# Optimization experiments

Hardware: AMD Instinct MI355X
Metric: run time of the kernel (lower is better)

The kernel has to match this reference:

```python
import jax, jax.numpy as jnp
import numpy as np

H = 128
N_CAN = 100000
N_FLAG = 50000
E = 600000
L = 500000


def _sage_conv(x_src, x_dst, edge_index, Wl, bl, Wr):
    # PyG SAGEConv (mean aggr): lin_l(mean_{j in N(i)} x_j) + lin_r(x_i)
    src, dst = edge_index[0], edge_index[1]
    msg = x_src[src]                                        # [E, H] gather
    n_dst = x_dst.shape[0]
    agg = jax.ops.segment_sum(msg, dst, num_segments=n_dst)  # [N_dst, H]
    cnt = jax.ops.segment_sum(jnp.ones((msg.shape[0],), msg.dtype), dst,
                              num_segments=n_dst)
    mean = agg / jnp.maximum(cnt, 1.0)[:, None]
    return mean @ Wl.T + bl + x_dst @ Wr.T


def setup_inputs() -> dict:
    key = jax.random.key(0)
    ks = jax.random.split(key, 16)
    s = 1.0 / np.sqrt(H)
    inp = {
        'can_node_id': jnp.arange(N_CAN, dtype=jnp.int64) if jax.config.jax_enable_x64 else jnp.arange(N_CAN, dtype=jnp.int32),
        'flag_node_id': jnp.arange(N_FLAG, dtype=jnp.int32),
        'edge_index_cf': jnp.stack([
            jax.random.randint(ks[0], (E,), 0, N_CAN),
            jax.random.randint(ks[1], (E,), 0, N_FLAG)]),
        'edge_index_fc': jnp.stack([
            jax.random.randint(ks[2], (E,), 0, N_FLAG),
            jax.random.randint(ks[3], (E,), 0, N_CAN)]),
        'edge_label_index': jnp.stack([
            jax.random.randint(ks[4], (L,), 0, N_CAN),
            jax.random.randint(ks[5], (L,), 0, N_FLAG)]),
        'can_emb': jax.random.normal(ks[6], (N_CAN, H), jnp.float32),
        'flag_emb': jax.random.normal(ks[7], (N_FLAG, H), jnp.float32),
        # SAGEConv for edge type CAN->flag (updates flag nodes)
        'Wl_cf': jax.random.normal(ks[8], (H, H), jnp.float32) * s,
        'bl_cf': jnp.zeros((H,), jnp.float32),
        'Wr_cf': jax.random.normal(ks[9], (H, H), jnp.float32) * s,
        # SAGEConv for edge type flag->CAN (updates CAN nodes)
        'Wl_fc': jax.random.normal(ks[10], (H, H), jnp.float32) * s,
        'bl_fc': jnp.zeros((H,), jnp.float32),
        'Wr_fc': jax.random.normal(ks[11], (H, H), jnp.float32) * s,
        # classifier MLP
        'W1': jax.random.normal(ks[12], (H, 2 * H), jnp.float32) * (1.0 / np.sqrt(2 * H)),
        'b1': jnp.zeros((H,), jnp.float32),
        'W2': jax.random.normal(ks[13], (1, H), jnp.float32) * s,
        'b2': jnp.zeros((1,), jnp.float32),
    }
    return inp


def reference(can_node_id, flag_node_id, edge_index_cf, edge_index_fc,
              edge_label_index, can_emb, flag_emb,
              Wl_cf, bl_cf, Wr_cf, Wl_fc, bl_fc, Wr_fc,
              W1, b1, W2, b2):
    # embedding lookups
    x_can = can_emb[can_node_id]    # [N_CAN, H]
    x_flag = flag_emb[flag_node_id]  # [N_FLAG, H]
    # to_hetero single SAGE layer + relu (dropout is identity in eval)
    upd_flag = jax.nn.relu(_sage_conv(x_can, x_flag, edge_index_cf, Wl_cf, bl_cf, Wr_cf))
    upd_can = jax.nn.relu(_sage_conv(x_flag, x_can, edge_index_fc, Wl_fc, bl_fc, Wr_fc))
    # link prediction classifier
    src = upd_can[edge_label_index[0]]   # [L, H]
    dst = upd_flag[edge_label_index[1]]  # [L, H]
    h = jax.nn.relu(jnp.concatenate([src, dst], axis=-1) @ W1.T + b1)
    out = h @ W2.T + b2
    return out.reshape(-1)
```

## Files before the change

### kernel.cpp

```cpp
#include <hip/hip_runtime.h>
#include <hip/hip_bf16.h>

#define H 128
#define BSH 8
#define MAXB 1024
#define PCH 4096
#define PIT (PCH / 256)

typedef __attribute__((ext_vector_type(8))) short short8;
typedef __attribute__((ext_vector_type(4))) short short4v;
typedef __attribute__((ext_vector_type(4))) float floatx4;
typedef unsigned short ushort_t;
typedef unsigned int uint_t;

__device__ __forceinline__ short f2bf(float f) {
    __hip_bfloat16 h = __float2bfloat16(f);
    return *reinterpret_cast<short*>(&h);
}
__device__ __forceinline__ float bflo(uint_t u) { return __uint_as_float(u << 16); }
__device__ __forceinline__ float bfhi(uint_t u) { return __uint_as_float(u & 0xFFFF0000u); }
__device__ __forceinline__ uint_t pack_bf2(float x, float y) {
    return (uint_t)(ushort_t)f2bf(x) | ((uint_t)(ushort_t)f2bf(y) << 16);
}
__device__ __forceinline__ void acc8(float* acc, uint4 r) {
    acc[0] += bflo(r.x); acc[1] += bfhi(r.x);
    acc[2] += bflo(r.y); acc[3] += bfhi(r.y);
    acc[4] += bflo(r.z); acc[5] += bfhi(r.z);
    acc[6] += bflo(r.w); acc[7] += bfhi(r.w);
}

__global__ __launch_bounds__(256)
void bucket_hist_cvt_kernel(const int* __restrict__ ei1, const int* __restrict__ ei2,
                            int E, int NF, int B, int* __restrict__ bcnt, int nbh,
                            const float* __restrict__ a, int n4a,
                            const float* __restrict__ b, int n4b,
                            ushort_t* __restrict__ da, ushort_t* __restrict__ db,
                            const float* __restrict__ Wl_cf, const float* __restrict__ Wr_cf,
                            const float* __restrict__ Wl_fc, const float* __restrict__ Wr_fc,
                            const float* __restrict__ W1, ushort_t* __restrict__ wb) {
    __shared__ int h[MAXB];
    int tid = threadIdx.x;
    if ((int)blockIdx.x < nbh) {
        for (int i = tid; i < B; i += 256) h[i] = 0;
        __syncthreads();
        int base = blockIdx.x * PCH;
        #pragma unroll 4
        for (int it = 0; it < PIT; ++it) {
            int t = base + it * 256 + tid;
            if (t < 2 * E) {
                int g = (t < E) ? ei1[E + t] : (ei2[E + t - E] + NF);
                atomicAdd(&h[g >> BSH], 1);
            }
        }
        __syncthreads();
        for (int i = tid; i < B; i += 256)
            if (h[i]) atomicAdd(&bcnt[i], h[i]);
        return;
    }
    int i = ((int)blockIdx.x - nbh) * 256 + tid;
    const float* src; ushort_t* dst; int k;
    if (i < n4a) { src = a; dst = da; k = i; }
    else if (i < n4a + n4b) { src = b; dst = db; k = i - n4a; }
    else {
        int idx = (i - n4a - n4b) * 4;
        if (idx >= 98304) return;
        int off;
        if      (idx < 16384) { src = Wl_cf; off = idx; }
        else if (idx < 32768) { src = Wr_cf; off = idx - 16384; }
        else if (idx < 49152) { src = Wl_fc; off = idx - 32768; }
        else if (idx < 65536) { src = Wr_fc; off = idx - 49152; }
        else                  { src = W1;    off = idx - 65536; }
        float4 v = *(const float4*)(src + off);
        short4v s;
        s[0] = f2bf(v.x); s[1] = f2bf(v.y); s[2] = f2bf(v.z); s[3] = f2bf(v.w);
        *(short4v*)(wb + idx) = s;
        return;
    }
    float4 v = ((const float4*)src)[k];
    short4v s;
    s[0] = f2bf(v.x); s[1] = f2bf(v.y); s[2] = f2bf(v.z); s[3] = f2bf(v.w);
    ((short4v*)dst)[k] = s;
}

__global__ __launch_bounds__(256)
void partition_kernel(const int* __restrict__ ei1, const int* __restrict__ ei2,
                      int E, int NF, int B, const int* __restrict__ bcnt,
                      int* __restrict__ bfront, uint_t* __restrict__ part) {
    __shared__ int h[MAXB];
    __shared__ int basex[MAXB];
    __shared__ int sdata[256];
    int tid = threadIdx.x;
    {
        int base4 = tid * 4;
        int v[4]; int s = 0;
        #pragma unroll
        for (int i = 0; i < 4; ++i) { int idx = base4 + i; v[i] = (idx < B) ? bcnt[idx] : 0; s += v[i]; }
        sdata[tid] = s;
        __syncthreads();
        for (int off = 1; off < 256; off <<= 1) {
            int t = (tid >= off) ? sdata[tid - off] : 0;
            __syncthreads();
            sdata[tid] += t;
            __syncthreads();
        }
        int excl = tid ? sdata[tid - 1] : 0;
        #pragma unroll
        for (int i = 0; i < 4; ++i) {
            int idx = base4 + i;
            if (idx < B) basex[idx] = excl;
            excl += v[i];
        }
    }
    for (int i = tid; i < B; i += 256) h[i] = 0;
    __syncthreads();

    int base = blockIdx.x * PCH;
    int pay[PIT]; int bkv[PIT]; int rv[PIT];
    #pragma unroll
    for (int it = 0; it < PIT; ++it) {
        int t = base + it * 256 + tid;
        bkv[it] = -1;
        if (t < 2 * E) {
            int g, s;
            if (t < E) { g = ei1[E + t]; s = ei1[t]; }
            else       { int e = t - E; g = ei2[E + e] + NF; s = ei2[e]; }
            int bk = g >> BSH;
            bkv[it] = bk;
            rv[it] = atomicAdd(&h[bk], 1);
            pay[it] = (int)(((uint_t)(g & 255) << 24) | (uint_t)s);
        }
    }
    __syncthreads();
    for (int i = tid; i < B; i += 256) {
        int c = h[i];
        if (c) basex[i] += atomicAdd(&bfront[i], c);
    }
    __syncthreads();
    #pragma unroll
    for (int it = 0; it < PIT; ++it) {
        if (bkv[it] >= 0)
            part[basex[bkv[it]] + rv[it]] = (uint_t)pay[it];
    }
}

__global__ __launch_bounds__(256)
void fine_bin_kernel(const int* __restrict__ bcnt, int B, int nTot, int E2,
                     const uint_t* __restrict__ part,
                     int* __restrict__ offs, int* __restrict__ bins) {
    __shared__ int cnt[256];
    __shared__ int sdata[256];
    __shared__ int excl[256];
    int b = blockIdx.x;
    int tid = threadIdx.x;
    {
        int partial = 0;
        for (int i = tid; i < b; i += 256) partial += bcnt[i];
        sdata[tid] = partial;
        __syncthreads();
        for (int off = 128; off > 0; off >>= 1) {
            if (tid < off) sdata[tid] += sdata[tid + off];
            __syncthreads();
        }
    }
    int seg0 = sdata[0];
    int seg1 = seg0 + bcnt[b];
    int gbase = b << BSH;
    __syncthreads();
    cnt[tid] = 0;
    __syncthreads();
    for (int k = seg0 + tid; k < seg1; k += 256)
        atomicAdd(&cnt[part[k] >> 24], 1);
    __syncthreads();
    sdata[tid] = cnt[tid];
    __syncthreads();
    for (int off = 1; off < 256; off <<= 1) {
        int t = (tid >= off) ? sdata[tid - off] : 0;
        __syncthreads();
        sdata[tid] += t;
        __syncthreads();
    }
    excl[tid] = tid ? sdata[tid - 1] : 0;
    int g = gbase + tid;
    if (g < nTot) offs[g] = seg0 + excl[tid];
    if (b == 0 && tid == 0) offs[nTot] = E2;
    cnt[tid] = 0;
    __syncthreads();
    for (int k = seg0 + tid; k < seg1; k += 256) {
        uint_t e = part[k];
        int l = (int)(e >> 24);
        int r = atomicAdd(&cnt[l], 1);
        bins[seg0 + excl[l] + r] = (int)(e & 0x00FFFFFFu);
    }
}

__global__ __launch_bounds__(256)
void gather_mean16_kernel(const int* __restrict__ offs, int nTotal, int split,
                          const int* __restrict__ bins,
                          const ushort_t* __restrict__ embA, ushort_t* __restrict__ aggA,
                          const ushort_t* __restrict__ embB, ushort_t* __restrict__ aggB) {
    int g = blockIdx.x * 16 + (threadIdx.x >> 4);
    if (g >= nTotal) return;
    int l15 = threadIdx.x & 15;
    int start = offs[g];
    int end = offs[g + 1];
    int deg = end - start;
    const ushort_t* emb; ushort_t* agg; int row;
    if (g < split) { emb = embA; agg = aggA; row = g; }
    else           { emb = embB; agg = aggB; row = g - split; }

    float acc[8];
    #pragma unroll
    for (int t = 0; t < 8; ++t) acc[t] = 0.f;

    const ushort_t* ep = emb + l15 * 8;
    int nPre = deg < 16 ? deg : 16;
    int pre = (l15 < nPre) ? bins[start + l15] : 0;

    int k = 0;
    for (; k + 3 < nPre; k += 4) {
        int s0 = __shfl(pre, k,     16);
        int s1 = __shfl(pre, k + 1, 16);
        int s2 = __shfl(pre, k + 2, 16);
        int s3 = __shfl(pre, k + 3, 16);
        uint4 r0 = *(const uint4*)(ep + (size_t)s0 * H);
        uint4 r1 = *(const uint4*)(ep + (size_t)s1 * H);
        uint4 r2 = *(const uint4*)(ep + (size_t)s2 * H);
        uint4 r3 = *(const uint4*)(ep + (size_t)s3 * H);
        acc8(acc, r0); acc8(acc, r1); acc8(acc, r2); acc8(acc, r3);
    }
    for (; k < nPre; ++k) {
        int s = __shfl(pre, k, 16);
        uint4 r = *(const uint4*)(ep + (size_t)s * H);
        acc8(acc, r);
    }
    for (int kk = start + 16; kk < end; ++kk) {
        int s = bins[kk];
        uint4 r = *(const uint4*)(ep + (size_t)s * H);
        acc8(acc, r);
    }

    float inv = 1.0f / fmaxf((float)deg, 1.0f);
    uint4 o;
    o.x = pack_bf2(acc[0] * inv, acc[1] * inv);
    o.y = pack_bf2(acc[2] * inv, acc[3] * inv);
    o.z = pack_bf2(acc[4] * inv, acc[5] * inv);
    o.w = pack_bf2(acc[6] * inv, acc[7] * inv);
    *(uint4*)(agg + (size_t)row * H + l15 * 8) = o;
}

__global__ __launch_bounds__(256)
void sage3_kernel(int nbF, int NF, int NC,
                  ushort_t* __restrict__ aggf, const ushort_t* __restrict__ embf,
                  ushort_t* __restrict__ aggc, const ushort_t* __restrict__ embc,
                  const ushort_t* __restrict__ wlf, const ushort_t* __restrict__ wrf,
                  const float* __restrict__ blf,
                  const ushort_t* __restrict__ wlc, const ushort_t* __restrict__ wrc,
                  const float* __restrict__ blc,
                  const ushort_t* __restrict__ W1) {
    __shared__ short A[64][136];
    bool isF = (int)blockIdx.x < nbF;
    int nrows = isF ? NF : NC;
    int rbase = (isF ? blockIdx.x : blockIdx.x - nbF) * 64;
    ushort_t* io = isF ? aggf : aggc;
    const ushort_t* emb = isF ? embf : embc;
    const ushort_t* Wl = isF ? wlf : wlc;
    const ushort_t* Wr = isF ? wrf : wrc;
    const float* bl = isF ? blf : blc;
    int koff = isF ? 128 : 0;

    int tid = threadIdx.x;
    int lane = tid & 63;
    int wv = tid >> 6;
    int l15 = lane & 15;
    int quad = lane >> 4;
    int nb0 = 32 * wv + l15;

    floatx4 acc[4][2];
    #pragma unroll
    for (int i = 0; i < 4; ++i)
        #pragma unroll
        for (int j = 0; j < 2; ++j)
            acc[i][j] = (floatx4){0.f, 0.f, 0.f, 0.f};

    float blv0 = bl[nb0];
    float blv1 = bl[nb0 + 16];

    for (int idx = tid; idx < 64 * 16; idx += 256) {
        int r = idx >> 4, c = idx & 15;
        int row = rbase + r;
        uint4 v = (uint4){0u, 0u, 0u, 0u};
        if (row < nrows) v = *(const uint4*)(io + (size_t)row * H + c * 8);
        *(uint4*)&A[r][c * 8] = v;
    }
    __syncthreads();
    #pragma unroll
    for (int ks = 0; ks < 4; ++ks) {
        int kb = ks * 32 + quad * 8;
        short8 b0 = *(const short8*)(Wl + (size_t)nb0 * H + kb);
        short8 b1 = *(const short8*)(Wl + (size_t)(nb0 + 16) * H + kb);
        #pragma unroll
        for (int mt = 0; mt < 4; ++mt) {
            short8 a = *(const short8*)&A[16 * mt + l15][kb];
            acc[mt][0] = __builtin_amdgcn_mfma_f32_16x16x32_bf16(a, b0, acc[mt][0], 0, 0, 0);
            acc[mt][1] = __builtin_amdgcn_mfma_f32_16x16x32_bf16(a, b1, acc[mt][1], 0, 0, 0);
        }
    }
    __syncthreads();

    for (int idx = tid; idx < 64 * 16; idx += 256) {
        int r = idx >> 4, c = idx & 15;
        int row = rbase + r;
        uint4 v = (uint4){0u, 0u, 0u, 0u};
        if (row < nrows) v = *(const uint4*)(emb + (size_t)row * H + c * 8);
        *(uint4*)&A[r][c * 8] = v;
    }
    __syncthreads();
    #pragma unroll
    for (int ks = 0; ks < 4; ++ks) {
        int kb = ks * 32 + quad * 8;
        short8 b0 = *(const short8*)(Wr + (size_t)nb0 * H + kb);
        short8 b1 = *(const short8*)(Wr + (size_t)(nb0 + 16) * H + kb);
        #pragma unroll
        for (int mt = 0; mt < 4; ++mt) {
            short8 a = *(const short8*)&A[16 * mt + l15][kb];
            acc[mt][0] = __builtin_amdgcn_mfma_f32_16x16x32_bf16(a, b0, acc[mt][0], 0, 0, 0);
            acc[mt][1] = __builtin_amdgcn_mfma_f32_16x16x32_bf16(a, b1, acc[mt][1], 0, 0, 0);
        }
    }
    __syncthreads();

    #pragma unroll
    for (int mt = 0; mt < 4; ++mt)
        #pragma unroll
        for (int nt = 0; nt < 2; ++nt) {
            float blv = nt ? blv1 : blv0;
            int colw = nb0 + 16 * nt;
            #pragma unroll
            for (int rg = 0; rg < 4; ++rg) {
                int row = 16 * mt + quad * 4 + rg;
                A[row][colw] = f2bf(fmaxf(acc[mt][nt][rg] + blv, 0.0f));
                acc[mt][nt][rg] = 0.0f;
            }
        }
    __syncthreads();

    const ushort_t* W1p = W1 + koff;
    #pragma unroll
    for (int ks = 0; ks < 4; ++ks) {
        int kb = ks * 32 + quad * 8;
        short8 b0 = *(const short8*)(W1p + (size_t)nb0 * 256 + kb);
        short8 b1 = *(const short8*)(W1p + (size_t)(nb0 + 16) * 256 + kb);
        #pragma unroll
        for (int mt = 0; mt < 4; ++mt) {
            short8 a = *(const short8*)&A[16 * mt + l15][kb];
            acc[mt][0] = __builtin_amdgcn_mfma_f32_16x16x32_bf16(a, b0, acc[mt][0], 0, 0, 0);
            acc[mt][1] = __builtin_amdgcn_mfma_f32_16x16x32_bf16(a, b1, acc[mt][1], 0, 0, 0);
        }
    }

    #pragma unroll
    for (int mt = 0; mt < 4; ++mt)
        #pragma unroll
        for (int rg = 0; rg < 4; ++rg) {
            int row = rbase + 16 * mt + quad * 4 + rg;
            if (row < nrows) {
                io[(size_t)row * H + nb0]      = (ushort_t)f2bf(acc[mt][0][rg]);
                io[(size_t)row * H + nb0 + 16] = (ushort_t)f2bf(acc[mt][1][rg]);
            }
        }
}

__global__ __launch_bounds__(256)
void hist2_kernel(const int* __restrict__ ei1, const int* __restrict__ ei2, int E,
                  int* __restrict__ deg1, int* __restrict__ deg2) {
    int t = blockIdx.x * 256 + threadIdx.x;
    if (t < E) atomicAdd(&deg1[ei1[E + t]], 1);
    else if (t < 2 * E) { int e = t - E; atomicAdd(&deg2[ei2[E + e]], 1); }
}

__global__ __launch_bounds__(256)
void scan_blocksum_kernel(const int* __restrict__ deg, int n, int* __restrict__ bsums) {
    __shared__ int sdata[256];
    int tid = threadIdx.x;
    int base = blockIdx.x * 1024 + tid * 4;
    int v = 0;
    #pragma unroll
    for (int i = 0; i < 4; ++i) { int idx = base + i; if (idx < n) v += deg[idx]; }
    sdata[tid] = v;
    __syncthreads();
    for (int off = 128; off > 0; off >>= 1) {
        if (tid < off) sdata[tid] += sdata[tid + off];
        __syncthreads();
    }
    if (tid == 0) bsums[blockIdx.x] = sdata[0];
}

__global__ __launch_bounds__(256)
void scan_write_kernel(int* __restrict__ data, int n, const int* __restrict__ bsums) {
    __shared__ int sdata[256];
    __shared__ int boff;
    int tid = threadIdx.x;
    if (tid < 64) {
        int acc = 0;
        for (int i = tid; i < (int)blockIdx.x; i += 64) acc += bsums[i];
        #pragma unroll
        for (int off = 32; off > 0; off >>= 1) acc += __shfl_xor(acc, off, 64);
        if (tid == 0) boff = acc;
    }
    int base = blockIdx.x * 1024 + tid * 4;
    int v[4]; int s = 0;
    #pragma unroll
    for (int i = 0; i < 4; ++i) { int idx = base + i; v[i] = (idx < n) ? data[idx] : 0; s += v[i]; }
    sdata[tid] = s;
    __syncthreads();
    for (int off = 1; off < 256; off <<= 1) {
        int t = (tid >= off) ? sdata[tid - off] : 0;
        __syncthreads();
        sdata[tid] += t;
        __syncthreads();
    }
    int excl = (tid == 0 ? 0 : sdata[tid - 1]) + boff;
    #pragma unroll
    for (int i = 0; i < 4; ++i) {
        int idx = base + i;
        if (idx < n) data[idx] = excl;
        excl += v[i];
    }
}

__global__ __launch_bounds__(256)
void incl_to_start_kernel(const int* __restrict__ incl, int nTot, int* __restrict__ offs) {
    int g = blockIdx.x * 256 + threadIdx.x;
    if (g < nTot) offs[g + 1] = incl[g];
    if (g == 0) offs[0] = 0;
}

__global__ __launch_bounds__(256)
void bin2_kernel(const int* __restrict__ ei1, const int* __restrict__ ei2, int E,
                 int* __restrict__ offs1, int* __restrict__ offs2,
                 int* __restrict__ bins) {
    int t = blockIdx.x * 256 + threadIdx.x;
    if (t < E) {
        int pos = atomicAdd(&offs1[ei1[E + t]], 1);
        bins[pos] = ei1[t];
    } else if (t < 2 * E) {
        int e = t - E;
        int pos = atomicAdd(&offs2[ei2[E + e]], 1);
        bins[pos] = ei2[e];
    }
}

__global__ __launch_bounds__(256)
void classify_kernel(const int* __restrict__ eli, int L,
                     const ushort_t* __restrict__ u_can,
                     const ushort_t* __restrict__ u_flag,
                     const float* __restrict__ b1,
                     const float* __restrict__ W2,
                     const float* __restrict__ b2,
                     float* __restrict__ out) {
    int tid = threadIdx.x;
    int lane = tid & 63;
    int wv = tid >> 6;
    int sub = lane >> 4;
    int l15 = lane & 15;
    int p = blockIdx.x * 16 + wv * 4 + sub;
    if (p >= L) return;
    int i = eli[p];
    int j = eli[L + p];
    uint4 a = ((const uint4*)(u_can  + (size_t)i * H))[l15];
    uint4 b = ((const uint4*)(u_flag + (size_t)j * H))[l15];
    float4 bb0 = ((const float4*)b1)[l15 * 2];
    float4 bb1 = ((const float4*)b1)[l15 * 2 + 1];
    float4 w0  = ((const float4*)W2)[l15 * 2];
    float4 w1  = ((const float4*)W2)[l15 * 2 + 1];
    float s = fmaxf(bflo(a.x) + bflo(b.x) + bb0.x, 0.f) * w0.x
            + fmaxf(bfhi(a.x) + bfhi(b.x) + bb0.y, 0.f) * w0.y
            + fmaxf(bflo(a.y) + bflo(b.y) + bb0.z, 0.f) * w0.z
            + fmaxf(bfhi(a.y) + bfhi(b.y) + bb0.w, 0.f) * w0.w
            + fmaxf(bflo(a.z) + bflo(b.z) + bb1.x, 0.f) * w1.x
            + fmaxf(bfhi(a.z) + bfhi(b.z) + bb1.y, 0.f) * w1.y
            + fmaxf(bflo(a.w) + bflo(b.w) + bb1.z, 0.f) * w1.z
            + fmaxf(bfhi(a.w) + bfhi(b.w) + bb1.w, 0.f) * w1.w;
    #pragma unroll
    for (int off = 8; off > 0; off >>= 1)
        s += __shfl_down(s, off, 16);
    if (l15 == 0) out[p] = s + b2[0];
}

extern "C" void kernel_launch(void* const* d_in, const int* in_sizes, int n_in,
                              void* d_out, int out_size, void* d_ws, size_t ws_size,
                              hipStream_t stream) {
    const int*   ei_cf    = (const int*)d_in[2];
    const int*   ei_fc    = (const int*)d_in[3];
    const int*   eli      = (const int*)d_in[4];
    const float* can_emb  = (const float*)d_in[5];
    const float* flag_emb = (const float*)d_in[6];
    const float* Wl_cf    = (const float*)d_in[7];
    const float* bl_cf    = (const float*)d_in[8];
    const float* Wr_cf    = (const float*)d_in[9];
    const float* Wl_fc    = (const float*)d_in[10];
    const float* bl_fc    = (const float*)d_in[11];
    const float* Wr_fc    = (const float*)d_in[12];
    const float* W1       = (const float*)d_in[13];
    const float* b1       = (const float*)d_in[14];
    const float* W2       = (const float*)d_in[15];
    const float* b2       = (const float*)d_in[16];
    float* out = (float*)d_out;

    const int NCAN  = in_sizes[0];
    const int NFLAG = in_sizes[1];
    const int E     = in_sizes[2] / 2;
    const int L     = in_sizes[4] / 2;
    const int nTot  = NCAN + NFLAG;
    const int B     = (nTot + 255) >> BSH;

    ushort_t* aggc = (ushort_t*)d_ws;
    ushort_t* aggf = aggc + (size_t)NCAN * H;
    ushort_t* embc = aggf + (size_t)NFLAG * H;
    ushort_t* embf = embc + (size_t)NCAN * H;
    char* tail = (char*)(embf + (size_t)NFLAG * H);
    size_t tail_off = (size_t)(tail - (char*)d_ws);

    int nbF = (NFLAG + 63) / 64, nbC = (NCAN + 63) / 64;
    int n4c = NCAN * H / 4, n4f = NFLAG * H / 4;
    int nbcvt = (n4c + n4f + 24576 + 255) / 256;

    size_t off_offs  = tail_off;
    size_t off_bcnt  = off_offs  + (size_t)(nTot + 1) * 4;
    size_t off_bfrnt = off_bcnt  + (size_t)MAXB * 4;
    size_t off_bins  = off_bfrnt + (size_t)MAXB * 4;
    size_t off_part  = off_bins  + (size_t)2 * E * 4;
    size_t off_wb    = off_part  + (size_t)2 * E * 4;
    size_t need_new  = off_wb + 98304 * 2;

    int* offs   = (int*)((char*)d_ws + off_offs);
    int* bcnt   = (int*)((char*)d_ws + off_bcnt);
    int* bfront = (int*)((char*)d_ws + off_bfrnt);
    int* bins   = (int*)((char*)d_ws + off_bins);

    if (ws_size >= need_new && B <= MAXB) {
        uint_t* part = (uint_t*)((char*)d_ws + off_part);
        ushort_t* wb = (ushort_t*)((char*)d_ws + off_wb);
        ushort_t* wb_wlcf = wb, *wb_wrcf = wb + 16384, *wb_wlfc = wb + 32768,
                 *wb_wrfc = wb + 49152, *wb_w1 = wb + 65536;

        int nbh = (2 * E + PCH - 1) / PCH;
        hipMemsetAsync(bcnt, 0, (size_t)2 * MAXB * 4, stream);
        bucket_hist_cvt_kernel<<<nbh + nbcvt, 256, 0, stream>>>(
            ei_cf, ei_fc, E, NFLAG, B, bcnt, nbh,
            can_emb, n4c, flag_emb, n4f, embc, embf,
            Wl_cf, Wr_cf, Wl_fc, Wr_fc, W1, wb);
        partition_kernel<<<nbh, 256, 0, stream>>>(ei_cf, ei_fc, E, NFLAG, B, bcnt, bfront, part);
        fine_bin_kernel<<<B, 256, 0, stream>>>(bcnt, B, nTot, 2 * E, part, offs, bins);
        gather_mean16_kernel<<<(nTot + 15) / 16, 256, 0, stream>>>(
            offs, nTot, NFLAG, bins, embc, aggf, embf, aggc);
        sage3_kernel<<<nbF + nbC, 256, 0, stream>>>(
            nbF, NFLAG, NCAN, aggf, embf, aggc, embc,
            wb_wlcf, wb_wrcf, bl_cf, wb_wlfc, wb_wrfc, bl_fc, wb_w1);
    } else {
        int* scanf_ = bins;
        int* scanc_ = scanf_ + NFLAG;
        int* bins2  = scanc_ + NCAN;
        int* bsums  = bins2 + 2 * E;
        ushort_t* wb = (ushort_t*)(bsums + 256);
        ushort_t* wb_wlcf = wb, *wb_wrcf = wb + 16384, *wb_wlfc = wb + 32768,
                 *wb_wrfc = wb + 49152, *wb_w1 = wb + 65536;

        bucket_hist_cvt_kernel<<<nbcvt, 256, 0, stream>>>(
            ei_cf, ei_fc, E, NFLAG, B, bcnt, 0,
            can_emb, n4c, flag_emb, n4f, embc, embf,
            Wl_cf, Wr_cf, Wl_fc, Wr_fc, W1, wb);
        hipMemsetAsync(scanf_, 0, ((size_t)NFLAG + NCAN) * 4, stream);
        int nb = (nTot + 1023) / 1024;
        hist2_kernel<<<(2 * E + 255) / 256, 256, 0, stream>>>(ei_cf, ei_fc, E, scanf_, scanc_);
        scan_blocksum_kernel<<<nb, 256, 0, stream>>>(scanf_, nTot, bsums);
        scan_write_kernel<<<nb, 256, 0, stream>>>(scanf_, nTot, bsums);
        bin2_kernel<<<(2 * E + 255) / 256, 256, 0, stream>>>(ei_cf, ei_fc, E, scanf_, scanc_, bins2);
        incl_to_start_kernel<<<(nTot + 255) / 256, 256, 0, stream>>>(scanf_, nTot, offs);
        gather_mean16_kernel<<<(nTot + 15) / 16, 256, 0, stream>>>(
            offs, nTot, NFLAG, bins2, embc, aggf, embf, aggc);
        sage3_kernel<<<nbF + nbC, 256, 0, stream>>>(
            nbF, NFLAG, NCAN, aggf, embf, aggc, embc,
            wb_wlcf, wb_wrcf, bl_cf, wb_wlfc, wb_wrfc, bl_fc, wb_w1);
    }

    classify_kernel<<<(L + 15) / 16, 256, 0, stream>>>(
        eli, L, aggc, aggf, b1, W2, b2, out);
}
```

Before: 308.7 us.

## Fuse neighbor mean aggregation into SAGE GEMM kernel via shared memory

Removes the separate gather_mean16 kernel. Each sage block now gathers and averages neighbor embeddings for its own 64 rows and writes the bf16 means straight into shared memory before the MFMA GEMM. This drops a kernel launch and the global write and re-read of the aggregated tensor. In exchange, the gather runs with a block count of only N/64 and feeds the GEMM phase directly, which may cut latency hiding for the irregular gathers.

```diff
diff --git a/kernel.cpp b/kernel.cpp
--- a/kernel.cpp
+++ b/kernel.cpp
@@ -194,64 +194,10 @@
 }
 
 __global__ __launch_bounds__(256)
-void gather_mean16_kernel(const int* __restrict__ offs, int nTotal, int split,
-                          const int* __restrict__ bins,
-                          const ushort_t* __restrict__ embA, ushort_t* __restrict__ aggA,
-                          const ushort_t* __restrict__ embB, ushort_t* __restrict__ aggB) {
-    int g = blockIdx.x * 16 + (threadIdx.x >> 4);
-    if (g >= nTotal) return;
-    int l15 = threadIdx.x & 15;
-    int start = offs[g];
-    int end = offs[g + 1];
-    int deg = end - start;
-    const ushort_t* emb; ushort_t* agg; int row;
-    if (g < split) { emb = embA; agg = aggA; row = g; }
-    else           { emb = embB; agg = aggB; row = g - split; }
-
-    float acc[8];
-    #pragma unroll
-    for (int t = 0; t < 8; ++t) acc[t] = 0.f;
-
-    const ushort_t* ep = emb + l15 * 8;
-    int nPre = deg < 16 ? deg : 16;
-    int pre = (l15 < nPre) ? bins[start + l15] : 0;
-
-    int k = 0;
-    for (; k + 3 < nPre; k += 4) {
-        int s0 = __shfl(pre, k,     16);
-        int s1 = __shfl(pre, k + 1, 16);
-        int s2 = __shfl(pre, k + 2, 16);
-        int s3 = __shfl(pre, k + 3, 16);
-        uint4 r0 = *(const uint4*)(ep + (size_t)s0 * H);
-        uint4 r1 = *(const uint4*)(ep + (size_t)s1 * H);
-        uint4 r2 = *(const uint4*)(ep + (size_t)s2 * H);
-        uint4 r3 = *(const uint4*)(ep + (size_t)s3 * H);
-        acc8(acc, r0); acc8(acc, r1); acc8(acc, r2); acc8(acc, r3);
-    }
-    for (; k < nPre; ++k) {
-        int s = __shfl(pre, k, 16);
-        uint4 r = *(const uint4*)(ep + (size_t)s * H);
-        acc8(acc, r);
-    }
-    for (int kk = start + 16; kk < end; ++kk) {
-        int s = bins[kk];
-        uint4 r = *(const uint4*)(ep + (size_t)s * H);
-        acc8(acc, r);
-    }
-
-    float inv = 1.0f / fmaxf((float)deg, 1.0f);
-    uint4 o;
-    o.x = pack_bf2(acc[0] * inv, acc[1] * inv);
-    o.y = pack_bf2(acc[2] * inv, acc[3] * inv);
-    o.z = pack_bf2(acc[4] * inv, acc[5] * inv);
-    o.w = pack_bf2(acc[6] * inv, acc[7] * inv);
-    *(uint4*)(agg + (size_t)row * H + l15 * 8) = o;
-}
-
-__global__ __launch_bounds__(256)
-void sage3_kernel(int nbF, int NF, int NC,
-                  ushort_t* __restrict__ aggf, const ushort_t* __restrict__ embf,
-                  ushort_t* __restrict__ aggc, const ushort_t* __restrict__ embc,
+void sage4_kernel(int nbF, int NF, int NC,
+                  const int* __restrict__ offs, const int* __restrict__ bins,
+                  ushort_t* __restrict__ outf, const ushort_t* __restrict__ embf,
+                  ushort_t* __restrict__ outc, const ushort_t* __restrict__ embc,
                   const ushort_t* __restrict__ wlf, const ushort_t* __restrict__ wrf,
                   const float* __restrict__ blf,
                   const ushort_t* __restrict__ wlc, const ushort_t* __restrict__ wrc,
@@ -261,12 +207,14 @@
     bool isF = (int)blockIdx.x < nbF;
     int nrows = isF ? NF : NC;
     int rbase = (isF ? blockIdx.x : blockIdx.x - nbF) * 64;
-    ushort_t* io = isF ? aggf : aggc;
-    const ushort_t* emb = isF ? embf : embc;
+    ushort_t* io = isF ? outf : outc;
+    const ushort_t* embS = isF ? embf : embc;
+    const ushort_t* embN = isF ? embc : embf;
     const ushort_t* Wl = isF ? wlf : wlc;
     const ushort_t* Wr = isF ? wrf : wrc;
     const float* bl = isF ? blf : blc;
     int koff = isF ? 128 : 0;
+    int gofs = isF ? 0 : NF;
 
     int tid = threadIdx.x;
     int lane = tid & 63;
@@ -275,6 +223,59 @@
     int quad = lane >> 4;
     int nb0 = 32 * wv + l15;
 
+    float blv0 = bl[nb0];
+    float blv1 = bl[nb0 + 16];
+
+    {
+        const ushort_t* epN = embN + l15 * 8;
+        #pragma unroll
+        for (int it = 0; it < 4; ++it) {
+            int r = wv * 16 + it * 4 + quad;
+            int row = rbase + r;
+            int start = 0, end = 0;
+            if (row < nrows) { int g = gofs + row; start = offs[g]; end = offs[g + 1]; }
+            int deg = end - start;
+
+            float acc[8];
+            #pragma unroll
+            for (int t = 0; t < 8; ++t) acc[t] = 0.f;
+
+            int nPre = deg < 16 ? deg : 16;
+            int pre = (l15 < nPre) ? bins[start + l15] : 0;
+
+            int k = 0;
+            for (; k + 3 < nPre; k += 4) {
+                int s0 = __shfl(pre, k,     16);
+                int s1 = __shfl(pre, k + 1, 16);
+                int s2 = __shfl(pre, k + 2, 16);
+                int s3 = __shfl(pre, k + 3, 16);
+                uint4 r0 = *(const uint4*)(epN + (size_t)s0 * H);
+                uint4 r1 = *(const uint4*)(epN + (size_t)s1 * H);
+                uint4 r2 = *(const uint4*)(epN + (size_t)s2 * H);
+                uint4 r3 = *(const uint4*)(epN + (size_t)s3 * H);
+                acc8(acc, r0); acc8(acc, r1); acc8(acc, r2); acc8(acc, r3);
+            }
+            for (; k < nPre; ++k) {
+                int s = __shfl(pre, k, 16);
+                uint4 rr = *(const uint4*)(epN + (size_t)s * H);
+                acc8(acc, rr);
+            }
+            for (int kk = start + 16; kk < end; ++kk) {
+                int s = bins[kk];
+                uint4 rr = *(const uint4*)(epN + (size_t)s * H);
+                acc8(acc, rr);
+            }
+
+            float inv = 1.0f / fmaxf((float)deg, 1.0f);
+            uint4 o;
+            o.x = pack_bf2(acc[0] * inv, acc[1] * inv);
+            o.y = pack_bf2(acc[2] * inv, acc[3] * inv);
+            o.z = pack_bf2(acc[4] * inv, acc[5] * inv);
+            o.w = pack_bf2(acc[6] * inv, acc[7] * inv);
+            *(uint4*)&A[r][l15 * 8] = o;
+        }
+    }
+
     floatx4 acc[4][2];
     #pragma unroll
     for (int i = 0; i < 4; ++i)
@@ -282,16 +283,6 @@
         for (int j = 0; j < 2; ++j)
             acc[i][j] = (floatx4){0.f, 0.f, 0.f, 0.f};
 
-    float blv0 = bl[nb0];
-    float blv1 = bl[nb0 + 16];
-
-    for (int idx = tid; idx < 64 * 16; idx += 256) {
-        int r = idx >> 4, c = idx & 15;
-        int row = rbase + r;
-        uint4 v = (uint4){0u, 0u, 0u, 0u};
-        if (row < nrows) v = *(const uint4*)(io + (size_t)row * H + c * 8);
-        *(uint4*)&A[r][c * 8] = v;
-    }
     __syncthreads();
     #pragma unroll
     for (int ks = 0; ks < 4; ++ks) {
@@ -307,11 +298,13 @@
     }
     __syncthreads();
 
-    for (int idx = tid; idx < 64 * 16; idx += 256) {
+    #pragma unroll
+    for (int j = 0; j < 4; ++j) {
+        int idx = tid + 256 * j;
         int r = idx >> 4, c = idx & 15;
         int row = rbase + r;
         uint4 v = (uint4){0u, 0u, 0u, 0u};
-        if (row < nrows) v = *(const uint4*)(emb + (size_t)row * H + c * 8);
+        if (row < nrows) v = *(const uint4*)(embS + (size_t)row * H + c * 8);
         *(uint4*)&A[r][c * 8] = v;
     }
     __syncthreads();
@@ -552,10 +545,9 @@
             Wl_cf, Wr_cf, Wl_fc, Wr_fc, W1, wb);
         partition_kernel<<<nbh, 256, 0, stream>>>(ei_cf, ei_fc, E, NFLAG, B, bcnt, bfront, part);
         fine_bin_kernel<<<B, 256, 0, stream>>>(bcnt, B, nTot, 2 * E, part, offs, bins);
-        gather_mean16_kernel<<<(nTot + 15) / 16, 256, 0, stream>>>(
-            offs, nTot, NFLAG, bins, embc, aggf, embf, aggc);
-        sage3_kernel<<<nbF + nbC, 256, 0, stream>>>(
-            nbF, NFLAG, NCAN, aggf, embf, aggc, embc,
+        sage4_kernel<<<nbF + nbC, 256, 0, stream>>>(
+            nbF, NFLAG, NCAN, offs, bins,
+            aggf, embf, aggc, embc,
             wb_wlcf, wb_wrcf, bl_cf, wb_wlfc, wb_wrfc, bl_fc, wb_w1);
     } else {
         int* scanf_ = bins;
@@ -577,10 +569,9 @@
         scan_write_kernel<<<nb, 256, 0, stream>>>(scanf_, nTot, bsums);
         bin2_kernel<<<(2 * E + 255) / 256, 256, 0, stream>>>(ei_cf, ei_fc, E, scanf_, scanc_, bins2);
         incl_to_start_kernel<<<(nTot + 255) / 256, 256, 0, stream>>>(scanf_, nTot, offs);
-        gather_mean16_kernel<<<(nTot + 15) / 16, 256, 0, stream>>>(
-            offs, nTot, NFLAG, bins2, embc, aggf, embf, aggc);
-        sage3_kernel<<<nbF + nbC, 256, 0, stream>>>(
-            nbF, NFLAG, NCAN, aggf, embf, aggc, embc,
+        sage4_kernel<<<nbF + nbC, 256, 0, stream>>>(
+            nbF, NFLAG, NCAN, offs, bins2,
+            aggf, embf, aggc, embc,
             wb_wlcf, wb_wrcf, bl_cf, wb_wlfc, wb_wrfc, bl_fc, wb_w1);
     }
 
```

Result: no change. 307.2 us (-0.5%).
